# Kernel optimization log

Measured on AMD Instinct MI355X. Metric: run time of the kernel, lower is better.

## Reference

```python
import jax, jax.numpy as jnp
import numpy as np
from jax import lax

SPIKE_RATE = 100.0
TIME_STEPS = 100
ADAPT_FACTOR = 0.95
REFRACTORY = 2.0
N_NEURONS = 256


def setup_inputs() -> dict:
    key = jax.random.key(0)
    x = jax.random.normal(jax.random.fold_in(key, 1), (32, 64), dtype=jnp.float32)
    centers = jnp.linspace(-1.0, 1.0, N_NEURONS).astype(jnp.float32)
    widths = jnp.full((N_NEURONS,), 0.2, dtype=jnp.float32)
    adaptation_state = jnp.ones((N_NEURONS,), dtype=jnp.float32)
    refractory_state = jnp.zeros((N_NEURONS,), dtype=jnp.float32)
    return {
        "x": x,
        "centers": centers,
        "widths": widths,
        "adaptation_state": adaptation_state,
        "refractory_state": refractory_state,
        "seed": 0,
    }


def reference(x, centers, widths, adaptation_state, refractory_state, seed):
    # x: [B, F]; centers/widths/states: [N]
    # Gaussian tuning-curve response: [B, F, N]
    d = x[:, :, None] - centers[None, None, :]
    response = jnp.exp(-(d * d) / (2.0 * widths * widths))
    # adaptation applied once with the initial buffer state (as in torch source)
    response = response * adaptation_state[None, None, :]
    spike_prob = response * (SPIKE_RATE / 1000.0)

    base_key = jax.random.key(seed)

    def step(carry, t):
        ref, adapt = carry  # each [N]
        k = jax.random.fold_in(base_key, t)
        r = jax.random.uniform(k, spike_prob.shape, dtype=spike_prob.dtype)
        can_spike = (ref == 0).astype(spike_prob.dtype)  # [N]
        spike_t = (r < spike_prob).astype(spike_prob.dtype) * can_spike[None, None, :]
        ref = jnp.maximum(ref - 1.0, 0.0)
        occurred = spike_t.sum(axis=(0, 1)) > 0  # [N]
        ref = ref + occurred.astype(ref.dtype) * REFRACTORY
        adapt = adapt * jnp.where(occurred, ADAPT_FACTOR, 1.0)
        return (ref, adapt), spike_t

    (_, _), spikes = lax.scan(step, (refractory_state, adaptation_state),
                              jnp.arange(TIME_STEPS))
    # spikes: [T, B, F, N] -> [B, F, N, T] to match torch.stack(..., dim=-1)
    return jnp.moveaxis(spikes, 0, -1)
```

## Files before the change

### kernel.cpp

```cpp
#include <hip/hip_runtime.h>
#include <stdint.h>

typedef unsigned long long u64;
typedef unsigned int u32;
typedef float f32x4 __attribute__((ext_vector_type(4)));

#define T_STEPS 100
#define NNEUR 256
#define NBF 2048
#define NELEM (NBF * NNEUR)
#define T_PER_BLK 4

__device__ __forceinline__ void tf2x32(u32 k0, u32 k1, u32& x0, u32& x1) {
  u32 k2 = k0 ^ k1 ^ 0x1BD11BDAu;
  x0 += k0; x1 += k1;
#define TFR(r) { x0 += x1; x1 = (x1 << (r)) | (x1 >> (32 - (r))); x1 ^= x0; }
  TFR(13) TFR(15) TFR(26) TFR(6)
  x0 += k1; x1 += k2 + 1u;
  TFR(17) TFR(29) TFR(16) TFR(24)
  x0 += k2; x1 += k0 + 2u;
  TFR(13) TFR(15) TFR(26) TFR(6)
  x0 += k0; x1 += k1 + 3u;
  TFR(17) TFR(29) TFR(16) TFR(24)
  x0 += k1; x1 += k2 + 4u;
  TFR(13) TFR(15) TFR(26) TFR(6)
  x0 += k2; x1 += k0 + 5u;
#undef TFR
}

__device__ __forceinline__ u32 rotl32(u32 x, int r) {
  return __builtin_amdgcn_alignbit(x, x, 32 - r);
}

__global__ void __launch_bounds__(256) kern_p(
    const float* __restrict__ x, const float* __restrict__ c,
    const float* __restrict__ w, const float* __restrict__ a,
    u32* __restrict__ thr9, u32* __restrict__ occ32) {
  int idx = blockIdx.x * 256 + threadIdx.x;
  int n = idx & 255, bf = idx >> 8;
  float d = x[bf] - c[n];
  float denom = (2.0f * w[n]) * w[n];
  float q = -(d * d) / denom;
  float e = (float)exp((double)q);
  float p = (e * a[n]) * 0.1f;
  thr9[idx] = ((u32)ceilf(p * 8388608.0f)) << 9;
  if (blockIdx.x == 0 && threadIdx.x < 200) {
    ((uint4*)occ32)[threadIdx.x] = make_uint4(0u, 0u, 0u, 0u);
  }
}

__global__ void __launch_bounds__(256, 4) kern_bits2(
    const u32* __restrict__ thr9,
    const int* __restrict__ seedp,
    u32* __restrict__ cmp32,
    u32* __restrict__ occ32) {
  const int t0 = blockIdx.x * T_PER_BLK;
  const int g = blockIdx.y;
  const int tid = threadIdx.x;
  const int oct = tid & 7;
  const int bfl = tid >> 3;
  const int bf = g * 32 + bfl;
  const u32 seed = (u32)seedp[0];
  const u32 base_i = (u32)(bf * 256 + oct * 32);

  u32 th[32];
  const uint4* tp = (const uint4*)(thr9 + base_i);
#pragma unroll
  for (int q = 0; q < 8; ++q) {
    uint4 v = tp[q];
    th[4*q] = v.x; th[4*q+1] = v.y; th[4*q+2] = v.z; th[4*q+3] = v.w;
  }

  u32* cmp_base = cmp32 + (u32)bf * (T_STEPS * 8) + oct;

#pragma unroll 1
  for (int tt = 0; tt < T_PER_BLK; ++tt) {
    const int t = t0 + tt;
    u32 K0 = 0u, K1 = (u32)t;
    tf2x32(0u, seed, K0, K1);
    const u32 K2 = K0 ^ K1 ^ 0x1BD11BDAu;
    const u32 I10 = K1;
    const u32 I11 = K2 + 1u;
    const u32 I20 = K2;
    const u32 I21 = K0 + 2u;
    const u32 I30 = K0;
    const u32 I31 = K1 + 3u;
    const u32 I40 = K1;
    const u32 I41 = K2 + 4u;
    const u32 I50 = K2;
    const u32 I51 = K0 + 5u;

    const u32 x1base = base_i + K1;
    const u32 x0base = x1base + K0;
    u32 word = 0u;
#pragma unroll
    for (int k = 31; k >= 0; --k) {
      u32 x1 = x1base + (u32)k;
      u32 x0 = x0base + (u32)k;
      x1 = rotl32(x1, 13); x1 ^= x0;
#define QR(r) { x0 += x1; x1 = rotl32(x1, r); x1 ^= x0; }
      QR(15) QR(26) QR(6)
      x0 += I10; x1 += I11;
      QR(17) QR(29) QR(16) QR(24)
      x0 += I20; x1 += I21;
      QR(13) QR(15) QR(26) QR(6)
      x0 += I30; x1 += I31;
      QR(17) QR(29) QR(16) QR(24)
      x0 += I40; x1 += I41;
      QR(13) QR(15) QR(26) QR(6)
      x0 += I50; x1 += I51;
#undef QR
      word = (word << 1) | ((x0 ^ x1) < th[k] ? 1u : 0u);
    }

    cmp_base[t * 8] = word;

    u32 o = word;
    o |= (u32)__shfl_xor((int)o, 8, 64);
    o |= (u32)__shfl_xor((int)o, 16, 64);
    o |= (u32)__shfl_xor((int)o, 32, 64);
    if ((tid & 63) < 8) atomicOr(&occ32[t * 8 + oct], o);
  }
}

__global__ void __launch_bounds__(256) kern_out2(
    const u32* __restrict__ cmp32,
    const u32* __restrict__ occ32,
    const float* __restrict__ ref0,
    float* __restrict__ out) {
  __shared__ u32 s_can[T_STEPS * 8];
  __shared__ u32 s[T_STEPS * 8];
  const int bf = blockIdx.x;
  const int tid = threadIdx.x;

  uint4 myc = make_uint4(0u, 0u, 0u, 0u);
  if (tid < 200) myc = ((const uint4*)(cmp32 + (u64)bf * (T_STEPS * 8)))[tid];

  if (tid < 200) ((uint4*)s)[tid] = ((const uint4*)occ32)[tid];
  __syncthreads();

  {
    const int n = tid, lane = n & 63, v = n >> 6;
    float ref = ref0[n];
    for (int t = 0; t < T_STEPS; ++t) {
      bool can = (ref == 0.0f);
      u64 cm = __ballot(can);
      if (lane == 0) {
        s_can[t * 8 + v * 2]     = (u32)cm;
        s_can[t * 8 + v * 2 + 1] = (u32)(cm >> 32);
      }
      bool occb = (s[t * 8 + (n >> 5)] >> (n & 31)) & 1u;
      bool occurred = can && occb;
      ref = fmaxf(ref - 1.0f, 0.0f) + (occurred ? 2.0f : 0.0f);
    }
  }
  __syncthreads();

  if (tid < 200) {
    uint4 cn = ((const uint4*)s_can)[tid];
    uint4 r;
    r.x = myc.x & cn.x; r.y = myc.y & cn.y;
    r.z = myc.z & cn.z; r.w = myc.w & cn.w;
    ((uint4*)s)[tid] = r;
  }
  __syncthreads();

  f32x4* outv = (f32x4*)(out + (u64)bf * (NNEUR * T_STEPS));
#pragma unroll
  for (int kk = 0; kk < 25; ++kk) {
    int q = tid + 256 * kk;
    int e = q * 4;
    f32x4 val;
#pragma unroll
    for (int j = 0; j < 4; ++j) {
      int ee = e + j;
      int n = ee / 100;
      int t = ee - n * 100;
      val[j] = (float)((s[t * 8 + (n >> 5)] >> (n & 31)) & 1u);
    }
    __builtin_nontemporal_store(val, &outv[q]);
  }
}

__global__ void __launch_bounds__(256) kern_bits_fb(
    const float* __restrict__ x, const float* __restrict__ c,
    const float* __restrict__ w, const float* __restrict__ a,
    const int* __restrict__ seedp,
    float* __restrict__ outf,
    u64* __restrict__ occ64) {
  const int t = blockIdx.x;
  const int chunk = blockIdx.y;
  const int lane = threadIdx.x & 63;
  const int v = threadIdx.x >> 6;
  const int n = v * 64 + lane;
  const u32 seed = (u32)seedp[0];
  u32 kt0 = 0u, kt1 = (u32)t;
  tf2x32(0u, seed, kt0, kt1);
  float cn = c[n], wn = w[n], an = a[n];
  bool occ = false;
  for (int j = 0; j < 64; ++j) {
    int bf = chunk * 64 + j;
    u32 i = (u32)(bf * 256 + n);
    u32 b0 = 0u, b1 = i;
    tf2x32(kt0, kt1, b0, b1);
    u32 bits = b0 ^ b1;
    float r = __uint_as_float((bits >> 9) | 0x3F800000u) - 1.0f;
    float d = x[bf] - cn;
    float denom = (2.0f * wn) * wn;
    float q = -(d * d) / denom;
    float pv = ((float)exp((double)q) * an) * 0.1f;
    bool cm = r < pv;
    occ |= cm;
    outf[(u64)bf * (NNEUR * T_STEPS) + (u64)n * T_STEPS + t] = cm ? 1.0f : 0.0f;
  }
  u64 om = __ballot(occ);
  if (lane == 0) atomicOr(&occ64[t * 4 + v], om);
}

__global__ void __launch_bounds__(256) kern_rec(
    const float* __restrict__ ref0,
    const u64* __restrict__ occ64,
    u64* __restrict__ can64) {
  int n = threadIdx.x;
  int lane = n & 63, v = n >> 6;
  float ref = ref0[n];
  for (int t = 0; t < T_STEPS; ++t) {
    bool can = (ref == 0.0f);
    u64 cm = __ballot(can);
    if (lane == 0) can64[t * 4 + v] = cm;
    bool occb = (occ64[t * 4 + v] >> lane) & 1ull;
    bool occurred = can && occb;
    ref = fmaxf(ref - 1.0f, 0.0f) + (occurred ? 2.0f : 0.0f);
  }
}

__global__ void __launch_bounds__(256) kern_mask(
    const u32* __restrict__ can32, float* __restrict__ out) {
  u64 q = (u64)blockIdx.x * 256 + threadIdx.x;
  float4* ov = (float4*)out;
  float4 vx = ov[q];
  u32 local = (u32)((q * 4) % (NNEUR * T_STEPS));
  float* vp = (float*)&vx;
#pragma unroll
  for (int j = 0; j < 4; ++j) {
    u32 le = local + j;
    u32 n = le / 100;
    u32 t = le - n * 100;
    u32 bit = (can32[t * 8 + (n >> 5)] >> (n & 31)) & 1u;
    vp[j] = bit ? vp[j] : 0.0f;
  }
  ov[q] = vx;
}

extern "C" void kernel_launch(void* const* d_in, const int* in_sizes, int n_in,
                              void* d_out, int out_size, void* d_ws, size_t ws_size,
                              hipStream_t stream) {
  const float* x  = (const float*)d_in[0];
  const float* c  = (const float*)d_in[1];
  const float* w  = (const float*)d_in[2];
  const float* a  = (const float*)d_in[3];
  const float* r0 = (const float*)d_in[4];
  const int* seed = (const int*)d_in[5];
  float* out = (float*)d_out;

  const size_t P_BYTES   = (size_t)NELEM * 4;
  const size_t CMP_BYTES = (size_t)NBF * T_STEPS * 4 * 8;
  const size_t OCC_BYTES = (size_t)T_STEPS * 4 * 8;
  const bool full = ws_size >= P_BYTES + CMP_BYTES + 2 * OCC_BYTES;

  uint8_t* wsb = (uint8_t*)d_ws;

  if (full) {
    u32* thr   = (u32*)wsb;
    u32* cmp   = (u32*)(wsb + P_BYTES);
    u32* occ   = (u32*)(wsb + P_BYTES + CMP_BYTES);
    kern_p<<<NELEM / 256, 256, 0, stream>>>(x, c, w, a, thr, occ);
    kern_bits2<<<dim3(T_STEPS / T_PER_BLK, 64), 256, 0, stream>>>(thr, seed, cmp, occ);
    kern_out2<<<NBF, 256, 0, stream>>>(cmp, occ, r0, out);
  } else {
    u64* occ = (u64*)wsb;
    u64* can = (u64*)(wsb + OCC_BYTES);
    hipMemsetAsync(occ, 0, OCC_BYTES, stream);
    kern_bits_fb<<<dim3(T_STEPS, 32), 256, 0, stream>>>(x, c, w, a, seed, out, occ);
    kern_rec<<<1, 256, 0, stream>>>(r0, occ, can);
    kern_mask<<<(out_size / 4) / 256, 256, 0, stream>>>((const u32*)can, out);
  }
}
```

Measured before the change: 379.5 us.

## Split RNG work to one timestep per block and transpose bit mask in LDS

The Threefry bit-generation kernel now runs one timestep per block and has each thread produce 16 comparison bits instead of 32. Neighbouring lanes merge their halves with a shuffle into full 32-bit words. This raises the block count and lowers per-thread register pressure (launch bounds now target 8 blocks per CU), meant to improve occupancy and latency hiding. The cost is more launches of the per-block key setup and threshold loads. The output kernel now stores the masked bits in LDS transposed as [word][t], so each float4 output element is built from one vector LDS read instead of four scattered reads with divisions.

```diff
diff --git a/kernel.cpp b/kernel.cpp
--- a/kernel.cpp
+++ b/kernel.cpp
@@ -9,7 +9,6 @@
 #define NNEUR 256
 #define NBF 2048
 #define NELEM (NBF * NNEUR)
-#define T_PER_BLK 4
 
 __device__ __forceinline__ void tf2x32(u32 k0, u32 k1, u32& x0, u32& x1) {
   u32 k2 = k0 ^ k1 ^ 0x1BD11BDAu;
@@ -49,94 +48,97 @@
   }
 }
 
-__global__ void __launch_bounds__(256, 4) kern_bits2(
+__global__ void __launch_bounds__(256, 8) kern_bits3(
     const u32* __restrict__ thr9,
     const int* __restrict__ seedp,
     u32* __restrict__ cmp32,
     u32* __restrict__ occ32) {
-  const int t0 = blockIdx.x * T_PER_BLK;
+  const int t = blockIdx.x;
   const int g = blockIdx.y;
   const int tid = threadIdx.x;
-  const int oct = tid & 7;
-  const int bfl = tid >> 3;
-  const int bf = g * 32 + bfl;
-  const u32 seed = (u32)seedp[0];
-  const u32 base_i = (u32)(bf * 256 + oct * 32);
-
-  u32 th[32];
+  const int hoct = tid & 15;
+  const int bfl = tid >> 4;
+  const int bf = g * 16 + bfl;
+  const u32 seed = (u32)__builtin_amdgcn_readfirstlane((int)seedp[0]);
+
+  u32 K0 = 0u, K1 = (u32)t;
+  tf2x32(0u, seed, K0, K1);
+  const u32 K2 = K0 ^ K1 ^ 0x1BD11BDAu;
+  const u32 I10 = K1;
+  const u32 I11 = K2 + 1u;
+  const u32 I20 = K2;
+  const u32 I21 = K0 + 2u;
+  const u32 I30 = K0;
+  const u32 I31 = K1 + 3u;
+  const u32 I40 = K1;
+  const u32 I41 = K2 + 4u;
+  const u32 I50 = K2;
+  const u32 I51 = K0 + 5u;
+
+  const u32 base_i = (u32)(bf * 256 + hoct * 16);
+
+  u32 th[16];
   const uint4* tp = (const uint4*)(thr9 + base_i);
 #pragma unroll
-  for (int q = 0; q < 8; ++q) {
+  for (int q = 0; q < 4; ++q) {
     uint4 v = tp[q];
     th[4*q] = v.x; th[4*q+1] = v.y; th[4*q+2] = v.z; th[4*q+3] = v.w;
   }
 
-  u32* cmp_base = cmp32 + (u32)bf * (T_STEPS * 8) + oct;
-
-#pragma unroll 1
-  for (int tt = 0; tt < T_PER_BLK; ++tt) {
-    const int t = t0 + tt;
-    u32 K0 = 0u, K1 = (u32)t;
-    tf2x32(0u, seed, K0, K1);
-    const u32 K2 = K0 ^ K1 ^ 0x1BD11BDAu;
-    const u32 I10 = K1;
-    const u32 I11 = K2 + 1u;
-    const u32 I20 = K2;
-    const u32 I21 = K0 + 2u;
-    const u32 I30 = K0;
-    const u32 I31 = K1 + 3u;
-    const u32 I40 = K1;
-    const u32 I41 = K2 + 4u;
-    const u32 I50 = K2;
-    const u32 I51 = K0 + 5u;
-
-    const u32 x1base = base_i + K1;
-    const u32 x0base = x1base + K0;
-    u32 word = 0u;
-#pragma unroll
-    for (int k = 31; k >= 0; --k) {
-      u32 x1 = x1base + (u32)k;
-      u32 x0 = x0base + (u32)k;
-      x1 = rotl32(x1, 13); x1 ^= x0;
+  const u32 x1base = base_i + K1;
+  const u32 x0base = x1base + K0;
+  u32 word = 0u;
+#pragma unroll
+  for (int k = 15; k >= 0; --k) {
+    u32 x1 = x1base + (u32)k;
+    u32 x0 = x0base + (u32)k;
+    x1 = rotl32(x1, 13); x1 ^= x0;
 #define QR(r) { x0 += x1; x1 = rotl32(x1, r); x1 ^= x0; }
-      QR(15) QR(26) QR(6)
-      x0 += I10; x1 += I11;
-      QR(17) QR(29) QR(16) QR(24)
-      x0 += I20; x1 += I21;
-      QR(13) QR(15) QR(26) QR(6)
-      x0 += I30; x1 += I31;
-      QR(17) QR(29) QR(16) QR(24)
-      x0 += I40; x1 += I41;
-      QR(13) QR(15) QR(26) QR(6)
-      x0 += I50; x1 += I51;
+    QR(15) QR(26) QR(6)
+    x0 += I10; x1 += I11;
+    QR(17) QR(29) QR(16) QR(24)
+    x0 += I20; x1 += I21;
+    QR(13) QR(15) QR(26) QR(6)
+    x0 += I30; x1 += I31;
+    QR(17) QR(29) QR(16) QR(24)
+    x0 += I40; x1 += I41;
+    QR(13) QR(15) QR(26) QR(6)
+    x0 += I50; x1 += I51;
 #undef QR
-      word = (word << 1) | ((x0 ^ x1) < th[k] ? 1u : 0u);
-    }
-
-    cmp_base[t * 8] = word;
-
-    u32 o = word;
-    o |= (u32)__shfl_xor((int)o, 8, 64);
-    o |= (u32)__shfl_xor((int)o, 16, 64);
-    o |= (u32)__shfl_xor((int)o, 32, 64);
-    if ((tid & 63) < 8) atomicOr(&occ32[t * 8 + oct], o);
-  }
-}
-
-__global__ void __launch_bounds__(256) kern_out2(
+    word = (word << 1) | ((x0 ^ x1) < th[k] ? 1u : 0u);
+  }
+
+  u32 partner = (u32)__shfl_xor((int)word, 1, 64);
+  if (!(hoct & 1)) {
+    u32 word32 = word | (partner << 16);
+    cmp32[(u32)bf * (T_STEPS * 8) + (u32)t * 8 + (hoct >> 1)] = word32;
+  }
+
+  u32 o = word;
+  o |= (u32)__shfl_xor((int)o, 16, 64);
+  o |= (u32)__shfl_xor((int)o, 32, 64);
+  u32 op = (u32)__shfl_xor((int)o, 1, 64);
+  if ((tid & 63) < 16 && !(hoct & 1)) {
+    atomicOr(&occ32[t * 8 + (hoct >> 1)], o | (op << 16));
+  }
+}
+
+__global__ void __launch_bounds__(256) kern_out3(
     const u32* __restrict__ cmp32,
     const u32* __restrict__ occ32,
     const float* __restrict__ ref0,
     float* __restrict__ out) {
+  __shared__ u32 s_occ[T_STEPS * 8];
   __shared__ u32 s_can[T_STEPS * 8];
-  __shared__ u32 s[T_STEPS * 8];
+  __shared__ u32 s[8 * T_STEPS];
   const int bf = blockIdx.x;
   const int tid = threadIdx.x;
 
   uint4 myc = make_uint4(0u, 0u, 0u, 0u);
-  if (tid < 200) myc = ((const uint4*)(cmp32 + (u64)bf * (T_STEPS * 8)))[tid];
-
-  if (tid < 200) ((uint4*)s)[tid] = ((const uint4*)occ32)[tid];
+  if (tid < 200) {
+    myc = ((const uint4*)(cmp32 + (u64)bf * (T_STEPS * 8)))[tid];
+    ((uint4*)s_occ)[tid] = ((const uint4*)occ32)[tid];
+  }
   __syncthreads();
 
   {
@@ -149,7 +151,7 @@
         s_can[t * 8 + v * 2]     = (u32)cm;
         s_can[t * 8 + v * 2 + 1] = (u32)(cm >> 32);
       }
-      bool occb = (s[t * 8 + (n >> 5)] >> (n & 31)) & 1u;
+      bool occb = (s_occ[t * 8 + (n >> 5)] >> (n & 31)) & 1u;
       bool occurred = can && occb;
       ref = fmaxf(ref - 1.0f, 0.0f) + (occurred ? 2.0f : 0.0f);
     }
@@ -157,11 +159,12 @@
   __syncthreads();
 
   if (tid < 200) {
-    uint4 cn = ((const uint4*)s_can)[tid];
-    uint4 r;
-    r.x = myc.x & cn.x; r.y = myc.y & cn.y;
-    r.z = myc.z & cn.z; r.w = myc.w & cn.w;
-    ((uint4*)s)[tid] = r;
+    const int t = tid >> 1, w0 = (tid & 1) * 4;
+    const u32* mp = (const u32*)&myc;
+#pragma unroll
+    for (int j = 0; j < 4; ++j) {
+      s[(w0 + j) * T_STEPS + t] = mp[j] & s_can[t * 8 + w0 + j];
+    }
   }
   __syncthreads();
 
@@ -170,14 +173,15 @@
   for (int kk = 0; kk < 25; ++kk) {
     int q = tid + 256 * kk;
     int e = q * 4;
+    int n = e / 100;
+    int t0 = e - n * 100;
+    int bit = n & 31;
+    uint4 wv = *(const uint4*)&s[(n >> 5) * T_STEPS + t0];
     f32x4 val;
-#pragma unroll
-    for (int j = 0; j < 4; ++j) {
-      int ee = e + j;
-      int n = ee / 100;
-      int t = ee - n * 100;
-      val[j] = (float)((s[t * 8 + (n >> 5)] >> (n & 31)) & 1u);
-    }
+    val[0] = (float)((wv.x >> bit) & 1u);
+    val[1] = (float)((wv.y >> bit) & 1u);
+    val[2] = (float)((wv.z >> bit) & 1u);
+    val[3] = (float)((wv.w >> bit) & 1u);
     __builtin_nontemporal_store(val, &outv[q]);
   }
 }
@@ -275,8 +279,8 @@
     u32* cmp   = (u32*)(wsb + P_BYTES);
     u32* occ   = (u32*)(wsb + P_BYTES + CMP_BYTES);
     kern_p<<<NELEM / 256, 256, 0, stream>>>(x, c, w, a, thr, occ);
-    kern_bits2<<<dim3(T_STEPS / T_PER_BLK, 64), 256, 0, stream>>>(thr, seed, cmp, occ);
-    kern_out2<<<NBF, 256, 0, stream>>>(cmp, occ, r0, out);
+    kern_bits3<<<dim3(T_STEPS, 128), 256, 0, stream>>>(thr, seed, cmp, occ);
+    kern_out3<<<NBF, 256, 0, stream>>>(cmp, occ, r0, out);
   } else {
     u64* occ = (u64*)wsb;
     u64* can = (u64*)(wsb + OCC_BYTES);
```

After: 336.0 us. -11.5%, faster.
